# Optimization experiments

Hardware: AMD Instinct MI355X
Metric: run time of the kernel (lower is better)

## Reference

```python
import jax, jax.numpy as jnp
import numpy as np

# RCGANConfig constants
D_X, D_EPS = 64, 16
A_VOCAB, A_EMB = 100, 32
T_VOCAB, T_EMB = 4, 16
D_H = 128
D_IN = A_EMB + T_EMB + D_X + D_EPS + 1  # 129 (use_prev_y adds 1)


def setup_inputs() -> dict:
    key = jax.random.key(0)
    ks = jax.random.split(key, 20)
    B, T = 1024, 256
    s = 0.05
    x = jax.random.normal(ks[0], (B, D_X), jnp.float32)
    a = jax.random.randint(ks[1], (B, T), 0, A_VOCAB, jnp.int32)
    t = jax.random.randint(ks[2], (B, T), 0, T_VOCAB, jnp.int32)
    y = (jax.random.uniform(ks[3], (B, T)) < 0.5).astype(jnp.float32)
    mask = jnp.ones((B, T), jnp.float32)
    eps = jax.random.normal(ks[4], (B, T, D_EPS), jnp.float32)
    # parameters
    Wx = jax.random.normal(ks[5], (D_X, D_X), jnp.float32) * s
    bx = jnp.zeros((D_X,), jnp.float32)
    Ea = jax.random.normal(ks[6], (A_VOCAB, A_EMB), jnp.float32) * s
    Et = jax.random.normal(ks[7], (T_VOCAB, T_EMB), jnp.float32) * s
    Wih = jax.random.normal(ks[8], (3 * D_H, D_IN), jnp.float32) * s
    Whh = jax.random.normal(ks[9], (3 * D_H, D_H), jnp.float32) * s
    bih = jnp.zeros((3 * D_H,), jnp.float32)
    bhh = jnp.zeros((3 * D_H,), jnp.float32)
    W0 = jax.random.normal(ks[10], (D_H, D_X + D_EPS), jnp.float32) * s
    b0 = jnp.zeros((D_H,), jnp.float32)
    Wy = jax.random.normal(ks[11], (1, D_H), jnp.float32) * s
    by = jnp.zeros((1,), jnp.float32)
    return {"x": x, "a": a, "t": t, "y": y, "mask": mask, "eps": eps,
            "Wx": Wx, "bx": bx, "Ea": Ea, "Et": Et, "Wih": Wih, "Whh": Whh,
            "bih": bih, "bhh": bhh, "W0": W0, "b0": b0, "Wy": Wy, "by": by}


def reference(x, a, t, y, mask, eps, Wx, bx, Ea, Et, Wih, Whh, bih, bhh, W0, b0, Wy, by):
    # teacher_forcing path, rnn='gru', use_prev_y=True, y provided, stochastic_y=False
    B, T = a.shape
    x_enc = x @ Wx.T + bx                                        # [B, d_x] (constant per step)
    h0 = jnp.tanh(jnp.concatenate([x_enc, eps[:, 0, :]], -1) @ W0.T + b0)  # [B, d_h]
    # prev_y: zeros at t=0, then detached teacher signal y[:, t-1]
    prev_y = jnp.concatenate(
        [jnp.zeros((B, 1), y.dtype), jax.lax.stop_gradient(y[:, :-1])], axis=1)[..., None]  # [B,T,1]
    a_enc = Ea[a]                                                # [B,T,a_emb]
    t_enc = Et[t]                                                # [B,T,t_emb]
    inp = jnp.concatenate(
        [a_enc, t_enc, jnp.broadcast_to(x_enc[:, None, :], (B, T, x_enc.shape[-1])), eps, prev_y],
        axis=-1)                                                 # [B,T,d_in]
    gates_x = inp @ Wih.T + bih                                  # [B,T,3*d_h] precomputed input gates

    def step(h, gx):
        gh = h @ Whh.T + bhh
        gx_r, gx_z, gx_n = jnp.split(gx, 3, axis=-1)
        gh_r, gh_z, gh_n = jnp.split(gh, 3, axis=-1)
        r = jax.nn.sigmoid(gx_r + gh_r)
        z = jax.nn.sigmoid(gx_z + gh_z)
        n = jnp.tanh(gx_n + r * gh_n)
        h_new = (1.0 - z) * n + z * h
        return h_new, h_new

    _, hs = jax.lax.scan(step, h0, jnp.swapaxes(gates_x, 0, 1))  # hs: [T,B,d_h]
    hs = jnp.swapaxes(hs, 0, 1)                                  # [B,T,d_h]
    logits = hs @ Wy.T + by                                      # [B,T,1]
    prob = jax.nn.sigmoid(logits)
    m = mask[..., None]
    logits_o = m * logits + (1.0 - m) * jax.lax.stop_gradient(logits)
    y_o = m * prob + (1.0 - m) * jax.lax.stop_gradient(prob)
    # stacked: [..., 0] = y_logits, [..., 1] = y
    return jnp.concatenate([logits_o, y_o], axis=-1)             # [B,T,2]
```

## Files before the change

### kernel.cpp

```cpp
#include <hip/hip_runtime.h>
#include <hip/hip_bf16.h>

typedef __attribute__((ext_vector_type(8))) short bfrag;
typedef __attribute__((ext_vector_type(4))) float ffrag;

#define NB 1024
#define NT 256

#define KSIG -1.44269504f
#define KTAN -2.88539008f

static __device__ __forceinline__ float fast_rcp(float x) { return __builtin_amdgcn_rcpf(x); }
static __device__ __forceinline__ float sigm(float x) {
  return fast_rcp(1.f + __builtin_amdgcn_exp2f(-1.44269504f * x));
}
static __device__ __forceinline__ float sigm_pre(float s) {
  return fast_rcp(1.f + __builtin_amdgcn_exp2f(s));
}
static __device__ __forceinline__ float tanh_pre(float s) {
  return __builtin_fmaf(2.f, fast_rcp(1.f + __builtin_amdgcn_exp2f(s)), -1.f);
}
static __device__ __forceinline__ float tanh_f(float x) {
  return __builtin_fmaf(2.f, fast_rcp(1.f + __builtin_amdgcn_exp2f(-2.88539008f * x)), -1.f);
}
static __device__ __forceinline__ float bf2f(__hip_bfloat16 v) { return __bfloat162float(v); }
static __device__ __forceinline__ short f2bs(float f) {
  __hip_bfloat16 h = __float2bfloat16(f);
  return *reinterpret_cast<short*>(&h);
}
static __device__ __forceinline__ void barrier_lgkm() {
  asm volatile("s_waitcnt lgkmcnt(0)\n\ts_barrier" ::: "memory");
}

__global__ __launch_bounds__(512, 2) void gru_kernel(
    const float* __restrict__ x,
    const int* __restrict__ a_ids,
    const int* __restrict__ t_ids,
    const float* __restrict__ y,
    const float* __restrict__ eps,
    const float* __restrict__ Wx,
    const float* __restrict__ bx,
    const float* __restrict__ Ea,
    const float* __restrict__ Et,
    const float* __restrict__ Wih,
    const float* __restrict__ Whh,
    const float* __restrict__ bih,
    const float* __restrict__ bhh,
    const float* __restrict__ W0,
    const float* __restrict__ b0g,
    const float* __restrict__ Wy,
    const float* __restrict__ by,
    float* __restrict__ out)
{
  __shared__ __align__(16) __hip_bfloat16 h_bf[2][16][136];
  __shared__ __align__(16) __hip_bfloat16 Ea_s[100][40];
  __shared__ __align__(16) __hip_bfloat16 Et_s[4][16];
  __shared__ float prevy_s[2][16];
  __shared__ float bsum_r[128], bsum_z[128], bihn_s[128], bhhn_s[128];
  __shared__ float wprev_s[384];
  __shared__ __align__(16) char uni[38912];
  unsigned short* id_s    = (unsigned short*)(uni);
  __hip_bfloat16* eps_ch  = (__hip_bfloat16*)(uni + 8192);
  float*          y_ch    = (float*)(uni + 32768);
  float*          out_b   = (float*)(uni + 34816);
  __hip_bfloat16* Wxb     = (__hip_bfloat16*)(uni);
  __hip_bfloat16* W0b     = (__hip_bfloat16*)(uni + 8192);
  float*          x_s     = (float*)(uni + 28672);
  float*          eps0s   = (float*)(uni + 32832);
  float*          xe_s    = (float*)(uni + 33920);
  float*          h0f     = (float*)(uni);

  const int tid = threadIdx.x;
  const int w = tid >> 6, l = tid & 63;
  const int lmod = l & 15, ldiv = l >> 4;
  const int i_own = 16 * w + lmod;
  const int b0 = blockIdx.x * 16;

  if (tid < 128) {
    bsum_r[tid] = KSIG * (bih[tid] + bhh[tid]);
    bsum_z[tid] = KSIG * (bih[128 + tid] + bhh[128 + tid]);
    bihn_s[tid] = KTAN * bih[256 + tid];
    bhhn_s[tid] = KTAN * bhh[256 + tid];
  }
  if (tid < 384) wprev_s[tid] = ((tid < 256) ? KSIG : KTAN) * Wih[tid * 129 + 128];
  for (int j = tid; j < 3200; j += 512) {
    int r = j >> 5, c = j & 31;
    Ea_s[r][c] = __float2bfloat16(Ea[j]);
  }
  if (tid < 64) ((__hip_bfloat16*)Et_s)[tid] = __float2bfloat16(Et[tid]);
  for (int j = tid; j < 4096; j += 512)  Wxb[j] = __float2bfloat16(Wx[j]);
  for (int j = tid; j < 10240; j += 512) W0b[j] = __float2bfloat16(W0[j]);
  for (int j = tid; j < 1024; j += 512) {
    int r = j >> 6, c = j & 63;
    x_s[r * 65 + c] = x[(b0 + r) * 64 + c];
  }
  if (tid < 256) {
    int r = tid >> 4, c = tid & 15;
    eps0s[r * 17 + c] = eps[((b0 + r) * NT) * 16 + c];
  }
  const float by_f = by[0];

  bfrag Bh[3][4], Bi[3][2];
  #pragma unroll
  for (int g = 0; g < 3; g++) {
    const float sg = (g < 2) ? KSIG : KTAN;
    int n = (g * 8 + w) * 16 + lmod;
    #pragma unroll
    for (int kc = 0; kc < 4; kc++) {
      int k = kc * 32 + ldiv * 8;
      const float* wh = Whh + n * 128 + k;
      float4 h0v = *reinterpret_cast<const float4*>(wh);
      float4 h1v = *reinterpret_cast<const float4*>(wh + 4);
      bfrag th = {f2bs(sg * h0v.x), f2bs(sg * h0v.y), f2bs(sg * h0v.z), f2bs(sg * h0v.w),
                  f2bs(sg * h1v.x), f2bs(sg * h1v.y), f2bs(sg * h1v.z), f2bs(sg * h1v.w)};
      Bh[g][kc] = th;
    }
    #pragma unroll
    for (int kc = 0; kc < 2; kc++) {
      bfrag ti;
      #pragma unroll
      for (int j = 0; j < 8; j++) {
        int dk = kc * 32 + ldiv * 8 + j;
        int col = dk < 48 ? dk : dk + 64;
        ti[j] = f2bs(sg * Wih[n * 129 + col]);
      }
      Bi[g][kc] = ti;
    }
  }
  bfrag Bl[4];
  if (w == 7) {
    #pragma unroll
    for (int kc = 0; kc < 4; kc++) {
      bfrag bt;
      #pragma unroll
      for (int j = 0; j < 8; j++)
        bt[j] = (lmod == 0) ? f2bs(Wy[kc * 32 + ldiv * 8 + j]) : (short)0;
      Bl[kc] = bt;
    }
  }
  __syncthreads();

  for (int j = tid; j < 1024; j += 512) {
    int r = j & 15, i = j >> 4;
    float acc = bx[i];
    #pragma unroll 8
    for (int k = 0; k < 64; k++) acc += x_s[r * 65 + k] * bf2f(Wxb[i * 64 + k]);
    xe_s[r * 65 + i] = acc;
    h_bf[1][r][i] = __float2bfloat16(acc);
  }
  __syncthreads();

  for (int j = tid; j < 2048; j += 512) {
    int r = j & 15, o = j >> 4;
    float acc = b0g[o];
    #pragma unroll 8
    for (int k = 0; k < 64; k++) acc += xe_s[r * 65 + k] * bf2f(W0b[o * 80 + k]);
    #pragma unroll
    for (int k = 0; k < 16; k++) acc += eps0s[r * 17 + k] * bf2f(W0b[o * 80 + 64 + k]);
    h0f[r * 128 + o] = tanh_f(acc);
  }

  ffrag gxc[3];
  {
    ffrag z = {0.f, 0.f, 0.f, 0.f};
    gxc[0] = z; gxc[1] = z; gxc[2] = z;
    #pragma unroll
    for (int kc = 0; kc < 2; kc++) {
      bfrag axd = *reinterpret_cast<const bfrag*>(&h_bf[1][lmod][kc * 32 + ldiv * 8]);
      #pragma unroll
      for (int g = 0; g < 3; g++) {
        const float sg = (g < 2) ? KSIG : KTAN;
        int n = (g * 8 + w) * 16 + lmod;
        const float* wi = Wih + n * 129 + 48 + kc * 32 + ldiv * 8;
        bfrag bt;
        #pragma unroll
        for (int j = 0; j < 8; j++) bt[j] = f2bs(sg * wi[j]);
        gxc[g] = __builtin_amdgcn_mfma_f32_16x16x32_bf16(axd, bt, gxc[g], 0, 0, 0);
      }
    }
    float brf = bsum_r[i_own], bzf = bsum_z[i_own], bn1 = bihn_s[i_own];
    #pragma unroll
    for (int q = 0; q < 4; q++) {
      gxc[0][q] += brf;
      gxc[1][q] += bzf;
      gxc[2][q] += bn1;
    }
  }
  __syncthreads();

  float h_reg[4];
  #pragma unroll
  for (int q = 0; q < 4; q++) {
    int row = ldiv * 4 + q;
    float hv = h0f[row * 128 + i_own];
    h_reg[q] = hv;
    h_bf[0][row][i_own] = __float2bfloat16(hv);
  }
  __syncthreads();

  for (int j = tid; j < 4096; j += 512) {
    int r = j >> 8, t = j & 255;
    unsigned short v = (unsigned short)(a_ids[(b0 + r) * NT + t] |
                                        (t_ids[(b0 + r) * NT + t] << 8));
    id_s[t * 16 + r] = v;
  }
  {
    int r = tid >> 5, sub = tid & 31;
    const float* p = eps + ((b0 + r) * NT) * 16 + sub * 8;
    float4 eA = *reinterpret_cast<const float4*>(p);
    float4 eB = *reinterpret_cast<const float4*>(p + 4);
    int toff = sub >> 1, c8 = (sub & 1) * 8;
    bfrag e = {f2bs(eA.x), f2bs(eA.y), f2bs(eA.z), f2bs(eA.w),
               f2bs(eB.x), f2bs(eB.y), f2bs(eB.z), f2bs(eB.w)};
    *reinterpret_cast<bfrag*>(&eps_ch[(toff * 16 + r) * 24 + c8]) = e;
    if (tid < 64) {
      int r2 = tid >> 2, s2 = tid & 3;
      float4 yv = *reinterpret_cast<const float4*>(y + (b0 + r2) * NT + s2 * 4);
      *reinterpret_cast<float4*>(&y_ch[r2 * 16 + s2 * 4]) = yv;
    }
  }
  if (tid < 16) prevy_s[0][tid] = 0.f;
  const float wpr = wprev_s[i_own], wpz = wprev_s[128 + i_own], wpn = wprev_s[256 + i_own];
  const float bn2 = bhhn_s[i_own];
  const char* const ea_base  = (const char*)Ea_s + ldiv * 16;
  const char* const et_base  = (const char*)Et_s + ldiv * 16;
  const char* const eps_base = (const char*)eps_ch + lmod * 48 + (ldiv - 2) * 16;
  __syncthreads();

  ffrag pa0 = gxc[0], pa1 = gxc[1], pa2 = gxc[2];
  {
    int id = id_s[lmod];
    int aid = id & 127, tv = id >> 8;
    bfrag axA = *reinterpret_cast<const bfrag*>(ea_base + aid * 80);
    const char* etp = et_base + tv * 32;
    const char* epp = eps_base;
    bfrag axB = *reinterpret_cast<const bfrag*>(ldiv < 2 ? etp : epp);
    pa0 = __builtin_amdgcn_mfma_f32_16x16x32_bf16(axA, Bi[0][0], pa0, 0, 0, 0);
    pa1 = __builtin_amdgcn_mfma_f32_16x16x32_bf16(axA, Bi[1][0], pa1, 0, 0, 0);
    pa2 = __builtin_amdgcn_mfma_f32_16x16x32_bf16(axA, Bi[2][0], pa2, 0, 0, 0);
    pa0 = __builtin_amdgcn_mfma_f32_16x16x32_bf16(axB, Bi[0][1], pa0, 0, 0, 0);
    pa1 = __builtin_amdgcn_mfma_f32_16x16x32_bf16(axB, Bi[1][1], pa1, 0, 0, 0);
    pa2 = __builtin_amdgcn_mfma_f32_16x16x32_bf16(axB, Bi[2][1], pa2, 0, 0, 0);
  }

  for (int t = 0; t < NT; t++) {
    const int buf = t & 1, nbuf = buf ^ 1;

    if ((t & 15) == 1 && t > 16 && tid < 128) {
      int fc = (t - 17) >> 4;
      int r = tid >> 3, k = tid & 7;
      int s = fc * 16 + 2 * k, slot = s & 31;
      float4 v;
      v.x = out_b[slot * 32 + r * 2];
      v.y = out_b[slot * 32 + r * 2 + 1];
      v.z = out_b[(slot + 1) * 32 + r * 2];
      v.w = out_b[(slot + 1) * 32 + r * 2 + 1];
      *reinterpret_cast<float4*>(out + ((b0 + r) * NT + s) * 2) = v;
    }

    const bool ck = ((t & 15) == 0) && (t + 16 < NT);
    float4 eA, eB, yv;
    const int cr = tid >> 5, csub = tid & 31;
    if (ck) {
      const float* p = eps + ((b0 + cr) * NT + t + 16) * 16 + csub * 8;
      eA = *reinterpret_cast<const float4*>(p);
      eB = *reinterpret_cast<const float4*>(p + 4);
      if (tid < 64) {
        int r2 = tid >> 2, s2 = tid & 3;
        yv = *reinterpret_cast<const float4*>(y + (b0 + r2) * NT + t + 16 + s2 * 4);
      }
    }

    ffrag anh, agl;
    #pragma unroll
    for (int q = 0; q < 4; q++) anh[q] = bn2;
    if (w == 7) {
      #pragma unroll
      for (int q = 0; q < 4; q++) agl[q] = by_f;
    }
    #pragma unroll
    for (int kc = 0; kc < 4; kc++) {
      bfrag ah = *reinterpret_cast<const bfrag*>(&h_bf[buf][lmod][kc * 32 + ldiv * 8]);
      pa0 = __builtin_amdgcn_mfma_f32_16x16x32_bf16(ah, Bh[0][kc], pa0, 0, 0, 0);
      pa1 = __builtin_amdgcn_mfma_f32_16x16x32_bf16(ah, Bh[1][kc], pa1, 0, 0, 0);
      anh = __builtin_amdgcn_mfma_f32_16x16x32_bf16(ah, Bh[2][kc], anh, 0, 0, 0);
      if (w == 7)
        agl = __builtin_amdgcn_mfma_f32_16x16x32_bf16(ah, Bl[kc], agl, 0, 0, 0);
    }

    if (tid >= 384 && tid < 400) {
      int r = tid - 384;
      prevy_s[nbuf][r] = y_ch[((t >> 4) & 1) * 256 + r * 16 + (t & 15)];
    }

    if (w == 7 && t > 0 && lmod == 0) {
      int slot = (t - 1) & 31;
      #pragma unroll
      for (int q = 0; q < 4; q++) {
        int row = ldiv * 4 + q;
        float lg = agl[q];
        out_b[slot * 32 + row * 2]     = lg;
        out_b[slot * 32 + row * 2 + 1] = sigm(lg);
      }
    }

    #pragma unroll
    for (int q = 0; q < 4; q++) {
      int row = ldiv * 4 + q;
      float py = prevy_s[buf][row];
      float rv = sigm_pre(__builtin_fmaf(py, wpr, pa0[q]));
      float zv = sigm_pre(__builtin_fmaf(py, wpz, pa1[q]));
      float nv = tanh_pre(__builtin_fmaf(rv, anh[q], __builtin_fmaf(py, wpn, pa2[q])));
      float hn = __builtin_fmaf(zv, h_reg[q] - nv, nv);
      h_reg[q] = hn;
      h_bf[nbuf][row][i_own] = __float2bfloat16(hn);
    }

    if (t + 1 < NT) {
      const int tn = t + 1;
      const int ebase = (((tn >> 4) & 1) * 16 + (tn & 15)) * 16;
      int id = id_s[tn * 16 + lmod];
      int aid = id & 127, tv = id >> 8;
      bfrag axA = *reinterpret_cast<const bfrag*>(ea_base + aid * 80);
      const char* etp = et_base + tv * 32;
      const char* epp = eps_base + ebase * 48;
      bfrag axB = *reinterpret_cast<const bfrag*>(ldiv < 2 ? etp : epp);
      pa0 = gxc[0]; pa1 = gxc[1]; pa2 = gxc[2];
      pa0 = __builtin_amdgcn_mfma_f32_16x16x32_bf16(axA, Bi[0][0], pa0, 0, 0, 0);
      pa1 = __builtin_amdgcn_mfma_f32_16x16x32_bf16(axA, Bi[1][0], pa1, 0, 0, 0);
      pa2 = __builtin_amdgcn_mfma_f32_16x16x32_bf16(axA, Bi[2][0], pa2, 0, 0, 0);
      pa0 = __builtin_amdgcn_mfma_f32_16x16x32_bf16(axB, Bi[0][1], pa0, 0, 0, 0);
      pa1 = __builtin_amdgcn_mfma_f32_16x16x32_bf16(axB, Bi[1][1], pa1, 0, 0, 0);
      pa2 = __builtin_amdgcn_mfma_f32_16x16x32_bf16(axB, Bi[2][1], pa2, 0, 0, 0);
    }

    if (ck) {
      int cb2 = ((t >> 4) + 1) & 1;
      int toff = csub >> 1, c8 = (csub & 1) * 8;
      bfrag e = {f2bs(eA.x), f2bs(eA.y), f2bs(eA.z), f2bs(eA.w),
                 f2bs(eB.x), f2bs(eB.y), f2bs(eB.z), f2bs(eB.w)};
      *reinterpret_cast<bfrag*>(&eps_ch[((cb2 * 16 + toff) * 16 + cr) * 24 + c8]) = e;
      if (tid < 64) {
        int r2 = tid >> 2, s2 = tid & 3;
        *reinterpret_cast<float4*>(&y_ch[cb2 * 256 + r2 * 16 + s2 * 4]) = yv;
      }
    }

    barrier_lgkm();
  }

  if (w == 7) {
    ffrag agl;
    #pragma unroll
    for (int q = 0; q < 4; q++) agl[q] = by_f;
    #pragma unroll
    for (int kc = 0; kc < 4; kc++) {
      bfrag ah = *reinterpret_cast<const bfrag*>(&h_bf[0][lmod][kc * 32 + ldiv * 8]);
      agl = __builtin_amdgcn_mfma_f32_16x16x32_bf16(ah, Bl[kc], agl, 0, 0, 0);
    }
    if (lmod == 0) {
      #pragma unroll
      for (int q = 0; q < 4; q++) {
        int row = ldiv * 4 + q;
        float lg = agl[q];
        out_b[31 * 32 + row * 2]     = lg;
        out_b[31 * 32 + row * 2 + 1] = sigm(lg);
      }
    }
  }
  __syncthreads();
  if (tid < 128) {
    int r = tid >> 3, k = tid & 7;
    int s = 240 + 2 * k, slot = s & 31;
    float4 v;
    v.x = out_b[slot * 32 + r * 2];
    v.y = out_b[slot * 32 + r * 2 + 1];
    v.z = out_b[(slot + 1) * 32 + r * 2];
    v.w = out_b[(slot + 1) * 32 + r * 2 + 1];
    *reinterpret_cast<float4*>(out + ((b0 + r) * NT + s) * 2) = v;
  }
}

extern "C" void kernel_launch(void* const* d_in, const int* in_sizes, int n_in,
                              void* d_out, int out_size, void* d_ws, size_t ws_size,
                              hipStream_t stream) {
  const float* x   = (const float*)d_in[0];
  const int*   a   = (const int*)d_in[1];
  const int*   tt  = (const int*)d_in[2];
  const float* y   = (const float*)d_in[3];
  const float* eps = (const float*)d_in[5];
  const float* Wx  = (const float*)d_in[6];
  const float* bx  = (const float*)d_in[7];
  const float* Ea  = (const float*)d_in[8];
  const float* Et  = (const float*)d_in[9];
  const float* Wih = (const float*)d_in[10];
  const float* Whh = (const float*)d_in[11];
  const float* bih = (const float*)d_in[12];
  const float* bhh = (const float*)d_in[13];
  const float* W0  = (const float*)d_in[14];
  const float* b0  = (const float*)d_in[15];
  const float* Wy  = (const float*)d_in[16];
  const float* by  = (const float*)d_in[17];
  float* out = (float*)d_out;

  gru_kernel<<<NB / 16, 512, 0, stream>>>(x, a, tt, y, eps, Wx, bx, Ea, Et,
                                          Wih, Whh, bih, bhh, W0, b0, Wy, by, out);
}
```

Before: 352.0 us.

## Write outputs directly, prefetch next-step input fragments early, and raise priority around recurrent MFMAs

Removes the LDS staging buffer for logits/probabilities and the periodic coalesced flushes; wave 7 now writes float2 results straight to global memory each step. The embedding and eps fragments for the next timestep are loaded from LDS at the top of the step so their latency overlaps the recurrent h·Whh MFMAs. s_setprio raises wave priority during the critical MFMA chain. The cost is scattered 8-byte global stores every step in place of batched float4 stores, plus extra live registers for the prefetched fragments.

```diff
diff --git a/kernel.cpp b/kernel.cpp
--- a/kernel.cpp
+++ b/kernel.cpp
@@ -62,7 +62,6 @@
   unsigned short* id_s    = (unsigned short*)(uni);
   __hip_bfloat16* eps_ch  = (__hip_bfloat16*)(uni + 8192);
   float*          y_ch    = (float*)(uni + 32768);
-  float*          out_b   = (float*)(uni + 34816);
   __hip_bfloat16* Wxb     = (__hip_bfloat16*)(uni);
   __hip_bfloat16* W0b     = (__hip_bfloat16*)(uni + 8192);
   float*          x_s     = (float*)(uni + 28672);
@@ -246,18 +245,6 @@
   for (int t = 0; t < NT; t++) {
     const int buf = t & 1, nbuf = buf ^ 1;
 
-    if ((t & 15) == 1 && t > 16 && tid < 128) {
-      int fc = (t - 17) >> 4;
-      int r = tid >> 3, k = tid & 7;
-      int s = fc * 16 + 2 * k, slot = s & 31;
-      float4 v;
-      v.x = out_b[slot * 32 + r * 2];
-      v.y = out_b[slot * 32 + r * 2 + 1];
-      v.z = out_b[(slot + 1) * 32 + r * 2];
-      v.w = out_b[(slot + 1) * 32 + r * 2 + 1];
-      *reinterpret_cast<float4*>(out + ((b0 + r) * NT + s) * 2) = v;
-    }
-
     const bool ck = ((t & 15) == 0) && (t + 16 < NT);
     float4 eA, eB, yv;
     const int cr = tid >> 5, csub = tid & 31;
@@ -271,6 +258,18 @@
       }
     }
 
+    bfrag axA_n, axB_n;
+    if (t + 1 < NT) {
+      const int tn = t + 1;
+      int id = id_s[tn * 16 + lmod];
+      int aid = id & 127, tv = id >> 8;
+      axA_n = *reinterpret_cast<const bfrag*>(ea_base + aid * 80);
+      const char* etp = et_base + tv * 32;
+      const int ebase2 = (((tn >> 4) & 1) * 16 + (tn & 15)) * 16;
+      const char* epp = eps_base + ebase2 * 48;
+      axB_n = *reinterpret_cast<const bfrag*>(ldiv < 2 ? etp : epp);
+    }
+
     ffrag anh, agl;
     #pragma unroll
     for (int q = 0; q < 4; q++) anh[q] = bn2;
@@ -278,6 +277,7 @@
       #pragma unroll
       for (int q = 0; q < 4; q++) agl[q] = by_f;
     }
+    __builtin_amdgcn_s_setprio(1);
     #pragma unroll
     for (int kc = 0; kc < 4; kc++) {
       bfrag ah = *reinterpret_cast<const bfrag*>(&h_bf[buf][lmod][kc * 32 + ldiv * 8]);
@@ -287,6 +287,7 @@
       if (w == 7)
         agl = __builtin_amdgcn_mfma_f32_16x16x32_bf16(ah, Bl[kc], agl, 0, 0, 0);
     }
+    __builtin_amdgcn_s_setprio(0);
 
     if (tid >= 384 && tid < 400) {
       int r = tid - 384;
@@ -294,13 +295,14 @@
     }
 
     if (w == 7 && t > 0 && lmod == 0) {
-      int slot = (t - 1) & 31;
       #pragma unroll
       for (int q = 0; q < 4; q++) {
         int row = ldiv * 4 + q;
         float lg = agl[q];
-        out_b[slot * 32 + row * 2]     = lg;
-        out_b[slot * 32 + row * 2 + 1] = sigm(lg);
+        float2 v;
+        v.x = lg;
+        v.y = sigm(lg);
+        *reinterpret_cast<float2*>(out + ((b0 + row) * NT + (t - 1)) * 2) = v;
       }
     }
 
@@ -317,21 +319,13 @@
     }
 
     if (t + 1 < NT) {
-      const int tn = t + 1;
-      const int ebase = (((tn >> 4) & 1) * 16 + (tn & 15)) * 16;
-      int id = id_s[tn * 16 + lmod];
-      int aid = id & 127, tv = id >> 8;
-      bfrag axA = *reinterpret_cast<const bfrag*>(ea_base + aid * 80);
-      const char* etp = et_base + tv * 32;
-      const char* epp = eps_base + ebase * 48;
-      bfrag axB = *reinterpret_cast<const bfrag*>(ldiv < 2 ? etp : epp);
       pa0 = gxc[0]; pa1 = gxc[1]; pa2 = gxc[2];
-      pa0 = __builtin_amdgcn_mfma_f32_16x16x32_bf16(axA, Bi[0][0], pa0, 0, 0, 0);
-      pa1 = __builtin_amdgcn_mfma_f32_16x16x32_bf16(axA, Bi[1][0], pa1, 0, 0, 0);
-      pa2 = __builtin_amdgcn_mfma_f32_16x16x32_bf16(axA, Bi[2][0], pa2, 0, 0, 0);
-      pa0 = __builtin_amdgcn_mfma_f32_16x16x32_bf16(axB, Bi[0][1], pa0, 0, 0, 0);
-      pa1 = __builtin_amdgcn_mfma_f32_16x16x32_bf16(axB, Bi[1][1], pa1, 0, 0, 0);
-      pa2 = __builtin_amdgcn_mfma_f32_16x16x32_bf16(axB, Bi[2][1], pa2, 0, 0, 0);
+      pa0 = __builtin_amdgcn_mfma_f32_16x16x32_bf16(axA_n, Bi[0][0], pa0, 0, 0, 0);
+      pa1 = __builtin_amdgcn_mfma_f32_16x16x32_bf16(axA_n, Bi[1][0], pa1, 0, 0, 0);
+      pa2 = __builtin_amdgcn_mfma_f32_16x16x32_bf16(axA_n, Bi[2][0], pa2, 0, 0, 0);
+      pa0 = __builtin_amdgcn_mfma_f32_16x16x32_bf16(axB_n, Bi[0][1], pa0, 0, 0, 0);
+      pa1 = __builtin_amdgcn_mfma_f32_16x16x32_bf16(axB_n, Bi[1][1], pa1, 0, 0, 0);
+      pa2 = __builtin_amdgcn_mfma_f32_16x16x32_bf16(axB_n, Bi[2][1], pa2, 0, 0, 0);
     }
 
     if (ck) {
@@ -363,21 +357,12 @@
       for (int q = 0; q < 4; q++) {
         int row = ldiv * 4 + q;
         float lg = agl[q];
-        out_b[31 * 32 + row * 2]     = lg;
-        out_b[31 * 32 + row * 2 + 1] = sigm(lg);
-      }
-    }
-  }
-  __syncthreads();
-  if (tid < 128) {
-    int r = tid >> 3, k = tid & 7;
-    int s = 240 + 2 * k, slot = s & 31;
-    float4 v;
-    v.x = out_b[slot * 32 + r * 2];
-    v.y = out_b[slot * 32 + r * 2 + 1];
-    v.z = out_b[(slot + 1) * 32 + r * 2];
-    v.w = out_b[(slot + 1) * 32 + r * 2 + 1];
-    *reinterpret_cast<float4*>(out + ((b0 + r) * NT + s) * 2) = v;
+        float2 v;
+        v.x = lg;
+        v.y = sigm(lg);
+        *reinterpret_cast<float2*>(out + ((b0 + row) * NT + 255) * 2) = v;
+      }
+    }
   }
 }
 
```

After: 363.5 us. +3.3%, slower.
